# Kernel tuning notes

Measured on AMD Instinct MI355X. Metric: run time of the kernel, lower is better.

Reference implementation:

```python
import jax, jax.numpy as jnp
import numpy as np

N_NODES = 50000
N_EDGES = 800000
H = 128
IN_DIM = 512
N_LAYERS = 3
LN_EPS = 1e-5


def setup_inputs() -> dict:
    key = jax.random.key(0)
    ks = jax.random.split(key, 12)
    s_in = 1.0 / np.sqrt(IN_DIM)
    s_h = 1.0 / np.sqrt(H)
    return {
        "peptide_feature": jax.random.normal(ks[0], (N_NODES, IN_DIM), jnp.float32),
        "proj_W": jax.random.uniform(ks[1], (IN_DIM, H), jnp.float32, -s_in, s_in),
        "proj_b": jax.random.uniform(ks[2], (H,), jnp.float32, -s_in, s_in),
        "edge_emb": jax.random.normal(ks[3], (100, H), jnp.float32),
        "conv_W1": jax.random.uniform(ks[4], (N_LAYERS, H, H), jnp.float32, -s_h, s_h),
        "conv_b1": jax.random.uniform(ks[5], (N_LAYERS, H), jnp.float32, -s_h, s_h),
        "conv_W2": jax.random.uniform(ks[6], (N_LAYERS, H, H), jnp.float32, -s_h, s_h),
        "conv_b2": jax.random.uniform(ks[7], (N_LAYERS, H), jnp.float32, -s_h, s_h),
        "ln_gamma": jnp.ones((H,), jnp.float32),
        "ln_beta": jnp.zeros((H,), jnp.float32),
        "edge_index": jax.random.randint(ks[8], (2, N_EDGES), 0, N_NODES, jnp.int64 if jax.config.jax_enable_x64 else jnp.int32),
        "edge_attr": jax.random.randint(ks[9], (N_EDGES, 1), 0, 100, jnp.int64 if jax.config.jax_enable_x64 else jnp.int32),
    }


def reference(peptide_feature, proj_W, proj_b, edge_emb, conv_W1, conv_b1,
              conv_W2, conv_b2, ln_gamma, ln_beta, edge_index, edge_attr):
    # aanet_proj: Linear(512, H)
    x = peptide_feature @ proj_W + proj_b  # [N, H]
    # edge type embedding lookup
    ea = edge_emb[edge_attr[:, 0]]  # [E, H]
    src, dst = edge_index[0], edge_index[1]
    n = x.shape[0]
    for i in range(N_LAYERS):
        # GINEConv (eps=0): aggr_i = sum_{(j->i)} relu(x_j + e_ji); out = MLP(x + aggr)
        msg = jax.nn.relu(x[src] + ea)  # [E, H] gather + add + relu
        agg = jax.ops.segment_sum(msg, dst, num_segments=n)  # scatter-add [N, H]
        h = x + agg
        h = jax.nn.relu(h @ conv_W1[i] + conv_b1[i]) @ conv_W2[i] + conv_b2[i]
        x = h + x  # residual
    # LayerNorm over last dim
    mu = jnp.mean(x, axis=-1, keepdims=True)
    var = jnp.var(x, axis=-1, keepdims=True)
    return ln_gamma * (x - mu) * jax.lax.rsqrt(var + LN_EPS) + ln_beta
```

## Files before the change

kernel.cpp:

```cpp
#include <hip/hip_runtime.h>
#include <hip/hip_bf16.h>

#define N_NODES 50000
#define N_EDGES 800000
#define H 128
#define IN_DIM 512
#define N_LAYERS 3
#define LN_EPS 1e-5f
#define SCAN_B ((N_NODES + 255) / 256)
#define BIN_CH 8192
#define BIN_BLOCKS ((N_EDGES + BIN_CH - 1) / BIN_CH)

typedef __attribute__((ext_vector_type(4))) float f32x4;
typedef __attribute__((ext_vector_type(8))) short short8;

__device__ inline ushort f2bfu(float f) {
    __hip_bfloat16 h = __float2bfloat16(f);
    return __builtin_bit_cast(ushort, h);
}
__device__ inline float bfu2f(ushort u) {
    uint v = ((uint)u) << 16;
    return __builtin_bit_cast(float, v);
}
__device__ inline float lobf(uint u) { return __builtin_bit_cast(float, u << 16); }
__device__ inline float hibf(uint u) { return __builtin_bit_cast(float, u & 0xffff0000u); }

#define SWZ(row, byte) ((byte) ^ (((row) & 7) << 4))

__device__ inline short8 cvt8(float4 a, float4 b) {
    short8 v;
    v[0] = (short)f2bfu(a.x); v[1] = (short)f2bfu(a.y);
    v[2] = (short)f2bfu(a.z); v[3] = (short)f2bfu(a.w);
    v[4] = (short)f2bfu(b.x); v[5] = (short)f2bfu(b.y);
    v[6] = (short)f2bfu(b.z); v[7] = (short)f2bfu(b.w);
    return v;
}


__global__ void hist_k(const int* __restrict__ dst, int* __restrict__ deg) {
    int e = blockIdx.x * 256 + threadIdx.x;
    if (e < N_EDGES) atomicAdd(&deg[dst[e]], 1);
}

__global__ __launch_bounds__(256) void blocksum_k(const int* __restrict__ deg,
                                                  int* __restrict__ bsum) {
    int i = blockIdx.x * 256 + threadIdx.x;
    int v = (i < N_NODES) ? deg[i] : 0;
    #pragma unroll
    for (int d = 1; d < 64; d <<= 1) v += __shfl_xor(v, d);
    __shared__ int ws[4];
    if ((threadIdx.x & 63) == 0) ws[threadIdx.x >> 6] = v;
    __syncthreads();
    if (threadIdx.x == 0) bsum[blockIdx.x] = ws[0] + ws[1] + ws[2] + ws[3];
}

__global__ __launch_bounds__(256) void scanb_k(const int* __restrict__ bsum,
                                               int* __restrict__ boff) {
    __shared__ int s[256];
    int t = threadIdx.x;
    int v = (t < SCAN_B) ? bsum[t] : 0;
    s[t] = v;
    __syncthreads();
    for (int d = 1; d < 256; d <<= 1) {
        int u = (t >= d) ? s[t - d] : 0;
        __syncthreads();
        s[t] += u;
        __syncthreads();
    }
    boff[t] = s[t] - v;
}

__global__ __launch_bounds__(256) void offs_k(const int* __restrict__ deg,
                                              const int* __restrict__ boff,
                                              int* __restrict__ offs,
                                              int* __restrict__ bbase,
                                              int* __restrict__ bcur) {
    int i = blockIdx.x * 256 + threadIdx.x;
    int lane = threadIdx.x & 63, w = threadIdx.x >> 6;
    int v = (i < N_NODES) ? deg[i] : 0;
    int inc = v;
    #pragma unroll
    for (int d = 1; d < 64; d <<= 1) {
        int u = __shfl_up(inc, d);
        if (lane >= d) inc += u;
    }
    __shared__ int wsum[4];
    if (lane == 63) wsum[w] = inc;
    __syncthreads();
    int wo = 0;
    #pragma unroll
    for (int k = 0; k < 4; k++) if (k < w) wo += wsum[k];
    int exc = boff[blockIdx.x] + wo + inc - v;
    if (i < N_NODES) offs[i] = exc;
    if ((i & 255) == 0 && i < N_NODES) { bbase[i >> 8] = exc; bcur[i >> 8] = exc; }
    if (i == N_NODES - 1) { offs[N_NODES] = exc + v; bbase[SCAN_B] = exc + v; }
}


__global__ __launch_bounds__(256) void binpass_k(const int* __restrict__ src,
                                                 const int* __restrict__ dst,
                                                 const int* __restrict__ attr,
                                                 int* __restrict__ bcur,
                                                 int* __restrict__ tmp_ep,
                                                 ushort* __restrict__ tmp_dst) {
    __shared__ int cnt[SCAN_B];
    __shared__ int lofs[SCAN_B];
    __shared__ int gbase[SCAN_B];
    __shared__ int cnt2[SCAN_B];
    __shared__ int scan_s[256];
    __shared__ int stage_ep[BIN_CH];
    __shared__ ushort stage_dst[BIN_CH];
    int tid = threadIdx.x;
    int e0 = blockIdx.x * BIN_CH;

    if (tid < SCAN_B) { cnt[tid] = 0; cnt2[tid] = 0; }
    __syncthreads();

    #pragma unroll
    for (int k = 0; k < BIN_CH / 256; k++) {
        int e = e0 + k * 256 + tid;
        if (e < N_EDGES) atomicAdd(&cnt[dst[e] >> 8], 1);
    }
    __syncthreads();

    int v = (tid < SCAN_B) ? cnt[tid] : 0;
    scan_s[tid] = v;
    __syncthreads();
    for (int d = 1; d < 256; d <<= 1) {
        int u = (tid >= d) ? scan_s[tid - d] : 0;
        __syncthreads();
        scan_s[tid] += u;
        __syncthreads();
    }
    if (tid < SCAN_B) lofs[tid] = scan_s[tid] - v;
    int total = scan_s[255];

    if (tid < SCAN_B && v > 0) gbase[tid] = atomicAdd(&bcur[tid], v);
    __syncthreads();

    #pragma unroll
    for (int k = 0; k < BIN_CH / 256; k++) {
        int e = e0 + k * 256 + tid;
        if (e < N_EDGES) {
            int d = dst[e];
            int b = d >> 8;
            int loc = lofs[b] + atomicAdd(&cnt2[b], 1);
            stage_ep[loc] = src[e] | (attr[e] << 16);
            stage_dst[loc] = (ushort)d;
        }
    }
    __syncthreads();

    for (int i = tid; i < total; i += 256) {
        ushort d = stage_dst[i];
        int b = d >> 8;
        int gp = gbase[b] + (i - lofs[b]);
        tmp_ep[gp] = stage_ep[i];
        tmp_dst[gp] = d;
    }
}


__global__ __launch_bounds__(256) void finepass_k(const int* __restrict__ tmp_ep,
                                                  const ushort* __restrict__ tmp_dst,
                                                  const int* __restrict__ offs,
                                                  const int* __restrict__ bbase,
                                                  int* __restrict__ epack) {
    __shared__ int cur[256];
    int tid = threadIdx.x;
    int node0 = blockIdx.x << 8;
    int node = node0 + tid;
    cur[tid] = (node < N_NODES) ? offs[node] : 0;
    __syncthreads();
    int lo = bbase[blockIdx.x], hi = bbase[blockIdx.x + 1];
    for (int i = lo + tid; i < hi; i += 256) {
        ushort d = tmp_dst[i];
        int ep = tmp_ep[i];
        int pos = atomicAdd(&cur[d & 255], 1);
        epack[pos] = ep;
    }
}


__global__ __launch_bounds__(256) void prep_w_k(const float* __restrict__ pW,
                                                const float* __restrict__ W1,
                                                const float* __restrict__ W2,
                                                const float* __restrict__ emb,
                                                short* __restrict__ Wt,
                                                short* __restrict__ W1t,
                                                short* __restrict__ W2t,
                                                ushort* __restrict__ embb,
                                                int* __restrict__ deg) {
    int i = blockIdx.x * 256 + threadIdx.x;
    if (i < 128 * 512) {
        int n = i >> 9, k = i & 511;
        Wt[i] = (short)f2bfu(pW[k * 128 + n]);
    }
    if (i < 3 * 128 * 128) {
        int l = i >> 14, rem = i & 16383, n = rem >> 7, k = rem & 127;
        W1t[i] = (short)f2bfu(W1[l * 16384 + k * 128 + n]);
        W2t[i] = (short)f2bfu(W2[l * 16384 + k * 128 + n]);
    }
    if (i < 100 * 128) embb[i] = f2bfu(emb[i]);
    if (i < N_NODES) deg[i] = 0;
}


__global__ __launch_bounds__(512) void proj_k(const float* __restrict__ pep,
                                              const short* __restrict__ Wt,
                                              const float* __restrict__ b,
                                              float* __restrict__ xf,
                                              ushort* __restrict__ xb) {
    __shared__ short SW[128 * 512];
    int tid = threadIdx.x, lane = tid & 63, wid = tid >> 6;

    #pragma unroll
    for (int c = 0; c < 16; c++) {
        int ch = tid + c * 512;
        int row = ch >> 6, kc = (ch & 63) * 16;
        short8 w = *(const short8*)((const char*)Wt + row * 1024 + kc);
        *(short8*)((char*)SW + SWZ(row, row * 1024 + kc)) = w;
    }
    __syncthreads();

    int m0 = blockIdx.x * 256 + wid * 32;

    const float* arow[2];
    #pragma unroll
    for (int mi = 0; mi < 2; mi++) {
        int node = m0 + mi * 16 + (lane & 15);
        if (node > N_NODES - 1) node = N_NODES - 1;
        arow[mi] = pep + (size_t)node * IN_DIM + ((lane >> 4) << 3);
    }

    f32x4 acc[2][8] = {};
    float4 A0[2][2], A1[2][2];
    #pragma unroll
    for (int mi = 0; mi < 2; mi++) {
        A0[mi][0] = *(const float4*)(arow[mi]);
        A0[mi][1] = *(const float4*)(arow[mi] + 4);
        A1[mi][0] = *(const float4*)(arow[mi] + 32);
        A1[mi][1] = *(const float4*)(arow[mi] + 36);
    }

    #pragma unroll
    for (int ks = 0; ks < 16; ks += 2) {
        {
            short8 af0 = cvt8(A0[0][0], A0[0][1]);
            short8 af1 = cvt8(A0[1][0], A0[1][1]);
            if (ks + 2 < 16) {
                #pragma unroll
                for (int mi = 0; mi < 2; mi++) {
                    A0[mi][0] = *(const float4*)(arow[mi] + (ks + 2) * 32);
                    A0[mi][1] = *(const float4*)(arow[mi] + (ks + 2) * 32 + 4);
                }
            }
            int kb2 = (ks * 32 + ((lane >> 4) << 3)) * 2;
            #pragma unroll
            for (int ni = 0; ni < 8; ni++) {
                int n = ni * 16 + (lane & 15);
                short8 bf = *(const short8*)((const char*)SW + SWZ(n, n * 1024 + kb2));
                acc[0][ni] = __builtin_amdgcn_mfma_f32_16x16x32_bf16(af0, bf, acc[0][ni], 0, 0, 0);
                acc[1][ni] = __builtin_amdgcn_mfma_f32_16x16x32_bf16(af1, bf, acc[1][ni], 0, 0, 0);
            }
        }
        {
            short8 af0 = cvt8(A1[0][0], A1[0][1]);
            short8 af1 = cvt8(A1[1][0], A1[1][1]);
            if (ks + 3 < 16) {
                #pragma unroll
                for (int mi = 0; mi < 2; mi++) {
                    A1[mi][0] = *(const float4*)(arow[mi] + (ks + 3) * 32);
                    A1[mi][1] = *(const float4*)(arow[mi] + (ks + 3) * 32 + 4);
                }
            }
            int kb2 = ((ks + 1) * 32 + ((lane >> 4) << 3)) * 2;
            #pragma unroll
            for (int ni = 0; ni < 8; ni++) {
                int n = ni * 16 + (lane & 15);
                short8 bf = *(const short8*)((const char*)SW + SWZ(n, n * 1024 + kb2));
                acc[0][ni] = __builtin_amdgcn_mfma_f32_16x16x32_bf16(af0, bf, acc[0][ni], 0, 0, 0);
                acc[1][ni] = __builtin_amdgcn_mfma_f32_16x16x32_bf16(af1, bf, acc[1][ni], 0, 0, 0);
            }
        }
    }

    #pragma unroll
    for (int ni = 0; ni < 8; ni++) {
        int col = ni * 16 + (lane & 15);
        float bb = b[col];
        #pragma unroll
        for (int mi = 0; mi < 2; mi++) {
            int rowb = m0 + mi * 16 + ((lane >> 4) << 2);
            #pragma unroll
            for (int r = 0; r < 4; r++) {
                int node = rowb + r;
                if (node < N_NODES) {
                    float v = acc[mi][ni][r] + bb;
                    xf[(size_t)node * H + col] = v;
                    xb[(size_t)node * H + col] = f2bfu(v);
                }
            }
        }
    }
}


__global__ __launch_bounds__(256) void gather_k(const ushort* __restrict__ xb,
                                                const int* __restrict__ offs,
                                                const int* __restrict__ epack,
                                                const ushort* __restrict__ embb,
                                                ushort* __restrict__ aggb) {
    int node = (blockIdx.x * 256 + threadIdx.x) >> 6;
    int lane = threadIdx.x & 63;
    if (node >= N_NODES) return;
    int beg = offs[node], end = offs[node + 1];
    float ax = 0.f, ay = 0.f;
    for (int base = beg; base < end; base += 64) {
        int myp = (base + lane < end) ? epack[base + lane] : 0;
        int cnt = min(64, end - base);
        int j = 0;
        for (; j + 4 <= cnt; j += 4) {
            int p0 = __shfl(myp, j), p1 = __shfl(myp, j + 1);
            int p2 = __shfl(myp, j + 2), p3 = __shfl(myp, j + 3);
            uint x0 = *(const uint*)(xb + (size_t)(p0 & 0xffff) * H + lane * 2);
            uint e0 = *(const uint*)(embb + (size_t)(p0 >> 16) * H + lane * 2);
            uint x1 = *(const uint*)(xb + (size_t)(p1 & 0xffff) * H + lane * 2);
            uint e1 = *(const uint*)(embb + (size_t)(p1 >> 16) * H + lane * 2);
            uint x2 = *(const uint*)(xb + (size_t)(p2 & 0xffff) * H + lane * 2);
            uint e2 = *(const uint*)(embb + (size_t)(p2 >> 16) * H + lane * 2);
            uint x3 = *(const uint*)(xb + (size_t)(p3 & 0xffff) * H + lane * 2);
            uint e3 = *(const uint*)(embb + (size_t)(p3 >> 16) * H + lane * 2);
            ax += fmaxf(lobf(x0) + lobf(e0), 0.f);
            ay += fmaxf(hibf(x0) + hibf(e0), 0.f);
            ax += fmaxf(lobf(x1) + lobf(e1), 0.f);
            ay += fmaxf(hibf(x1) + hibf(e1), 0.f);
            ax += fmaxf(lobf(x2) + lobf(e2), 0.f);
            ay += fmaxf(hibf(x2) + hibf(e2), 0.f);
            ax += fmaxf(lobf(x3) + lobf(e3), 0.f);
            ay += fmaxf(hibf(x3) + hibf(e3), 0.f);
        }
        for (; j < cnt; j++) {
            int p = __shfl(myp, j);
            uint xv = *(const uint*)(xb + (size_t)(p & 0xffff) * H + lane * 2);
            uint ev = *(const uint*)(embb + (size_t)(p >> 16) * H + lane * 2);
            ax += fmaxf(lobf(xv) + lobf(ev), 0.f);
            ay += fmaxf(hibf(xv) + hibf(ev), 0.f);
        }
    }
    uint packed = (uint)f2bfu(ax) | ((uint)f2bfu(ay) << 16);
    *(uint*)(aggb + (size_t)node * H + lane * 2) = packed;
}


#define MLP_ROWS 64
__global__ __launch_bounds__(256) void mlp_k(float* __restrict__ xf,
                                             ushort* __restrict__ xb,
                                             const ushort* __restrict__ aggb,
                                             const short* __restrict__ W1t,
                                             const float* __restrict__ b1,
                                             const short* __restrict__ W2t,
                                             const float* __restrict__ b2) {
    __shared__ short S[MLP_ROWS * 128];
    __shared__ short Wb[128 * 128];
    int tid = threadIdx.x, lane = tid & 63, wid = tid >> 6;
    int wr = wid >> 1, wc = wid & 1;
    int m0 = blockIdx.x * MLP_ROWS;

    #pragma unroll
    for (int c = 0; c < 4; c++) {
        int ch = tid + c * 256;
        int row = ch >> 4, k8 = (ch & 15) * 8;
        int node = m0 + row;
        short8 hv;
        if (node < N_NODES) {
            const float* xp = xf + (size_t)node * H + k8;
            float4 x0 = *(const float4*)xp;
            float4 x1 = *(const float4*)(xp + 4);
            short8 ag = *(const short8*)(aggb + (size_t)node * H + k8);
            hv[0] = (short)f2bfu(x0.x + bfu2f((ushort)ag[0]));
            hv[1] = (short)f2bfu(x0.y + bfu2f((ushort)ag[1]));
            hv[2] = (short)f2bfu(x0.z + bfu2f((ushort)ag[2]));
            hv[3] = (short)f2bfu(x0.w + bfu2f((ushort)ag[3]));
            hv[4] = (short)f2bfu(x1.x + bfu2f((ushort)ag[4]));
            hv[5] = (short)f2bfu(x1.y + bfu2f((ushort)ag[5]));
            hv[6] = (short)f2bfu(x1.z + bfu2f((ushort)ag[6]));
            hv[7] = (short)f2bfu(x1.w + bfu2f((ushort)ag[7]));
        } else {
            hv = (short8)0;
        }
        *(short8*)((char*)S + SWZ(row, row * 256 + k8 * 2)) = hv;
    }
    #pragma unroll
    for (int c = 0; c < 8; c++) {
        int ch = tid + c * 256;
        int row = ch >> 4, k8 = (ch & 15) * 8;
        short8 w = *(const short8*)(W1t + row * H + k8);
        *(short8*)((char*)Wb + SWZ(row, row * 256 + k8 * 2)) = w;
    }
    short8 wreg2[8];
    #pragma unroll
    for (int c = 0; c < 8; c++) {
        int ch = tid + c * 256;
        int row = ch >> 4, k8 = (ch & 15) * 8;
        wreg2[c] = *(const short8*)(W2t + row * H + k8);
    }
    __syncthreads();

    f32x4 a1[2][4] = {};
    #pragma unroll
    for (int ks = 0; ks < 4; ks++) {
        int kb = ks * 32 + (lane >> 4) * 8;
        short8 af[2], bfr[4];
        #pragma unroll
        for (int mi = 0; mi < 2; mi++) {
            int r = wr * 32 + mi * 16 + (lane & 15);
            af[mi] = *(const short8*)((const char*)S + SWZ(r, r * 256 + kb * 2));
        }
        #pragma unroll
        for (int ni = 0; ni < 4; ni++) {
            int n = wc * 64 + ni * 16 + (lane & 15);
            bfr[ni] = *(const short8*)((const char*)Wb + SWZ(n, n * 256 + kb * 2));
        }
        #pragma unroll
        for (int mi = 0; mi < 2; mi++)
            #pragma unroll
            for (int ni = 0; ni < 4; ni++)
                a1[mi][ni] = __builtin_amdgcn_mfma_f32_16x16x32_bf16(
                    af[mi], bfr[ni], a1[mi][ni], 0, 0, 0);
    }
    __syncthreads();

    #pragma unroll
    for (int ni = 0; ni < 4; ni++) {
        int n = wc * 64 + ni * 16 + (lane & 15);
        float bb = b1[n];
        #pragma unroll
        for (int mi = 0; mi < 2; mi++) {
            int mrow = wr * 32 + mi * 16 + ((lane >> 4) << 2);
            #pragma unroll
            for (int r = 0; r < 4; r++) {
                int m = mrow + r;
                float tv = fmaxf(a1[mi][ni][r] + bb, 0.f);
                *(ushort*)((char*)S + SWZ(m, m * 256 + n * 2)) = f2bfu(tv);
            }
        }
    }
    #pragma unroll
    for (int c = 0; c < 8; c++) {
        int ch = tid + c * 256;
        int row = ch >> 4, k8 = (ch & 15) * 8;
        *(short8*)((char*)Wb + SWZ(row, row * 256 + k8 * 2)) = wreg2[c];
    }
    __syncthreads();

    f32x4 a2[4][2] = {};
    #pragma unroll
    for (int ks = 0; ks < 4; ks++) {
        int kb = ks * 32 + (lane >> 4) * 8;
        short8 af[4], bfr[2];
        #pragma unroll
        for (int mi = 0; mi < 4; mi++) {
            int n2 = wr * 64 + mi * 16 + (lane & 15);
            af[mi] = *(const short8*)((const char*)Wb + SWZ(n2, n2 * 256 + kb * 2));
        }
        #pragma unroll
        for (int ni = 0; ni < 2; ni++) {
            int m = wc * 32 + ni * 16 + (lane & 15);
            bfr[ni] = *(const short8*)((const char*)S + SWZ(m, m * 256 + kb * 2));
        }
        #pragma unroll
        for (int mi = 0; mi < 4; mi++)
            #pragma unroll
            for (int ni = 0; ni < 2; ni++)
                a2[mi][ni] = __builtin_amdgcn_mfma_f32_16x16x32_bf16(
                    af[mi], bfr[ni], a2[mi][ni], 0, 0, 0);
    }

    #pragma unroll
    for (int ni = 0; ni < 2; ni++) {
        int node = m0 + wc * 32 + ni * 16 + (lane & 15);
        if (node >= N_NODES) continue;
        #pragma unroll
        for (int mi = 0; mi < 4; mi++) {
            int n2b = wr * 64 + mi * 16 + ((lane >> 4) << 2);
            float4 xo = *(float4*)(xf + (size_t)node * H + n2b);
            float4 bb = *(const float4*)(b2 + n2b);
            float4 o;
            o.x = a2[mi][ni][0] + bb.x + xo.x;
            o.y = a2[mi][ni][1] + bb.y + xo.y;
            o.z = a2[mi][ni][2] + bb.z + xo.z;
            o.w = a2[mi][ni][3] + bb.w + xo.w;
            *(float4*)(xf + (size_t)node * H + n2b) = o;
            ushort us[4] = {f2bfu(o.x), f2bfu(o.y), f2bfu(o.z), f2bfu(o.w)};
            *(ulong*)(xb + (size_t)node * H + n2b) = *(ulong*)us;
        }
    }
}


__global__ __launch_bounds__(256) void ln_k(const float* __restrict__ x,
                                            const float* __restrict__ gamma,
                                            const float* __restrict__ beta,
                                            float* __restrict__ out) {
    int node = (blockIdx.x * 256 + threadIdx.x) >> 6;
    int lane = threadIdx.x & 63;
    if (node >= N_NODES) return;
    float2 v = ((const float2*)(x + (size_t)node * H))[lane];
    float s = v.x + v.y;
    #pragma unroll
    for (int d = 1; d < 64; d <<= 1) s += __shfl_xor(s, d);
    float mu = s * (1.f / 128.f);
    float dx = v.x - mu, dy = v.y - mu;
    float q = dx * dx + dy * dy;
    #pragma unroll
    for (int d = 1; d < 64; d <<= 1) q += __shfl_xor(q, d);
    float inv = rsqrtf(q * (1.f / 128.f) + LN_EPS);
    float2 gm = ((const float2*)gamma)[lane];
    float2 bt = ((const float2*)beta)[lane];
    float2 o;
    o.x = gm.x * dx * inv + bt.x;
    o.y = gm.y * dy * inv + bt.y;
    ((float2*)(out + (size_t)node * H))[lane] = o;
}


extern "C" void kernel_launch(void* const* d_in, const int* in_sizes, int n_in,
                              void* d_out, int out_size, void* d_ws, size_t ws_size,
                              hipStream_t stream) {
    const float* pep    = (const float*)d_in[0];
    const float* proj_W = (const float*)d_in[1];
    const float* proj_b = (const float*)d_in[2];
    const float* emb    = (const float*)d_in[3];
    const float* cW1    = (const float*)d_in[4];
    const float* cb1    = (const float*)d_in[5];
    const float* cW2    = (const float*)d_in[6];
    const float* cb2    = (const float*)d_in[7];
    const float* gamma  = (const float*)d_in[8];
    const float* beta   = (const float*)d_in[9];
    const int*   eidx   = (const int*)d_in[10];
    const int*   attr   = (const int*)d_in[11];
    const int* src = eidx;
    const int* dst = eidx + N_EDGES;

    char* w = (char*)d_ws;
    float*  xf    = (float*)w;              w += (size_t)N_NODES * H * 4;
    ushort* xb    = (ushort*)w;             w += (size_t)N_NODES * H * 2;
    ushort* aggb  = (ushort*)w;             w += (size_t)N_NODES * H * 2;
    short*  Wt    = (short*)w;              w += 128 * 512 * 2;
    short*  W1t   = (short*)w;              w += 3 * 128 * 128 * 2;
    short*  W2t   = (short*)w;              w += 3 * 128 * 128 * 2;
    ushort* embb  = (ushort*)w;             w += 100 * 128 * 2;
    int*    offs  = (int*)w;                w += (N_NODES + 16) * 4;
    int*    deg   = (int*)w;                w += (N_NODES + 16) * 4;
    int*    bsum  = (int*)w;                w += 256 * 4;
    int*    boff  = (int*)w;                w += 256 * 4;
    int*    bbase = (int*)w;                w += 256 * 4;
    int*    bcur  = (int*)w;                w += 256 * 4;
    int*    epack = (int*)w;                w += (size_t)N_EDGES * 4;
    int*    tmp_ep = (int*)w;               w += (size_t)N_EDGES * 4;
    ushort* tmp_dst = (ushort*)w;           w += (size_t)N_EDGES * 2;

    float* out = (float*)d_out;

    prep_w_k<<<256, 256, 0, stream>>>(proj_W, cW1, cW2, emb, Wt, W1t, W2t, embb, deg);
    hist_k<<<(N_EDGES + 255) / 256, 256, 0, stream>>>(dst, deg);
    blocksum_k<<<SCAN_B, 256, 0, stream>>>(deg, bsum);
    scanb_k<<<1, 256, 0, stream>>>(bsum, boff);
    offs_k<<<SCAN_B, 256, 0, stream>>>(deg, boff, offs, bbase, bcur);
    binpass_k<<<BIN_BLOCKS, 256, 0, stream>>>(src, dst, attr, bcur, tmp_ep, tmp_dst);
    finepass_k<<<SCAN_B, 256, 0, stream>>>(tmp_ep, tmp_dst, offs, bbase, epack);

    proj_k<<<(N_NODES + 255) / 256, 512, 0, stream>>>(pep, Wt, proj_b, xf, xb);

    for (int l = 0; l < N_LAYERS; l++) {
        gather_k<<<(N_NODES * 64 + 255) / 256, 256, 0, stream>>>(
            xb, offs, epack, embb, aggb);
        mlp_k<<<(N_NODES + MLP_ROWS - 1) / MLP_ROWS, 256, 0, stream>>>(
            xf, xb, aggb,
            W1t + (size_t)l * H * H, cb1 + (size_t)l * H,
            W2t + (size_t)l * H * H, cb2 + (size_t)l * H);
    }

    ln_k<<<(N_NODES * 64 + 255) / 256, 256, 0, stream>>>(xf, gamma, beta, out);
}
```

Measured before the change: 305.5 us.

## Fuse neighbor gather-aggregation into MLP kernel with ping-pong bf16 buffers

Removes the separate gather kernel. Each MLP block now gathers and aggregates its own 64 nodes' neighbor messages and writes x+agg straight into shared memory, which avoids the round trip of the aggregate buffer through global memory and one launch per layer. Because other blocks still read the bf16 features of the current layer, the bf16 copy is double-buffered, and the final layer skips writing it. The cost is less parallelism for the irregular gather: one wave handles 16 nodes serially inside an MLP block with large shared memory, so occupancy and latency hiding for the gather may drop.

Measured after the change: 477.4 us. 56.3% more time.

```diff
diff --git a/kernel.cpp b/kernel.cpp
--- a/kernel.cpp
+++ b/kernel.cpp
@@ -306,61 +306,18 @@
 }
 
 
-__global__ __launch_bounds__(256) void gather_k(const ushort* __restrict__ xb,
-                                                const int* __restrict__ offs,
-                                                const int* __restrict__ epack,
-                                                const ushort* __restrict__ embb,
-                                                ushort* __restrict__ aggb) {
-    int node = (blockIdx.x * 256 + threadIdx.x) >> 6;
-    int lane = threadIdx.x & 63;
-    if (node >= N_NODES) return;
-    int beg = offs[node], end = offs[node + 1];
-    float ax = 0.f, ay = 0.f;
-    for (int base = beg; base < end; base += 64) {
-        int myp = (base + lane < end) ? epack[base + lane] : 0;
-        int cnt = min(64, end - base);
-        int j = 0;
-        for (; j + 4 <= cnt; j += 4) {
-            int p0 = __shfl(myp, j), p1 = __shfl(myp, j + 1);
-            int p2 = __shfl(myp, j + 2), p3 = __shfl(myp, j + 3);
-            uint x0 = *(const uint*)(xb + (size_t)(p0 & 0xffff) * H + lane * 2);
-            uint e0 = *(const uint*)(embb + (size_t)(p0 >> 16) * H + lane * 2);
-            uint x1 = *(const uint*)(xb + (size_t)(p1 & 0xffff) * H + lane * 2);
-            uint e1 = *(const uint*)(embb + (size_t)(p1 >> 16) * H + lane * 2);
-            uint x2 = *(const uint*)(xb + (size_t)(p2 & 0xffff) * H + lane * 2);
-            uint e2 = *(const uint*)(embb + (size_t)(p2 >> 16) * H + lane * 2);
-            uint x3 = *(const uint*)(xb + (size_t)(p3 & 0xffff) * H + lane * 2);
-            uint e3 = *(const uint*)(embb + (size_t)(p3 >> 16) * H + lane * 2);
-            ax += fmaxf(lobf(x0) + lobf(e0), 0.f);
-            ay += fmaxf(hibf(x0) + hibf(e0), 0.f);
-            ax += fmaxf(lobf(x1) + lobf(e1), 0.f);
-            ay += fmaxf(hibf(x1) + hibf(e1), 0.f);
-            ax += fmaxf(lobf(x2) + lobf(e2), 0.f);
-            ay += fmaxf(hibf(x2) + hibf(e2), 0.f);
-            ax += fmaxf(lobf(x3) + lobf(e3), 0.f);
-            ay += fmaxf(hibf(x3) + hibf(e3), 0.f);
-        }
-        for (; j < cnt; j++) {
-            int p = __shfl(myp, j);
-            uint xv = *(const uint*)(xb + (size_t)(p & 0xffff) * H + lane * 2);
-            uint ev = *(const uint*)(embb + (size_t)(p >> 16) * H + lane * 2);
-            ax += fmaxf(lobf(xv) + lobf(ev), 0.f);
-            ay += fmaxf(hibf(xv) + hibf(ev), 0.f);
-        }
-    }
-    uint packed = (uint)f2bfu(ax) | ((uint)f2bfu(ay) << 16);
-    *(uint*)(aggb + (size_t)node * H + lane * 2) = packed;
-}
-
-
 #define MLP_ROWS 64
 __global__ __launch_bounds__(256) void mlp_k(float* __restrict__ xf,
-                                             ushort* __restrict__ xb,
-                                             const ushort* __restrict__ aggb,
+                                             const ushort* __restrict__ xb_in,
+                                             ushort* __restrict__ xb_out,
+                                             const int* __restrict__ offs,
+                                             const int* __restrict__ epack,
+                                             const ushort* __restrict__ embb,
                                              const short* __restrict__ W1t,
                                              const float* __restrict__ b1,
                                              const short* __restrict__ W2t,
-                                             const float* __restrict__ b2) {
+                                             const float* __restrict__ b2,
+                                             int write_xb) {
     __shared__ short S[MLP_ROWS * 128];
     __shared__ short Wb[128 * 128];
     int tid = threadIdx.x, lane = tid & 63, wid = tid >> 6;
@@ -368,30 +325,6 @@
     int m0 = blockIdx.x * MLP_ROWS;
 
     #pragma unroll
-    for (int c = 0; c < 4; c++) {
-        int ch = tid + c * 256;
-        int row = ch >> 4, k8 = (ch & 15) * 8;
-        int node = m0 + row;
-        short8 hv;
-        if (node < N_NODES) {
-            const float* xp = xf + (size_t)node * H + k8;
-            float4 x0 = *(const float4*)xp;
-            float4 x1 = *(const float4*)(xp + 4);
-            short8 ag = *(const short8*)(aggb + (size_t)node * H + k8);
-            hv[0] = (short)f2bfu(x0.x + bfu2f((ushort)ag[0]));
-            hv[1] = (short)f2bfu(x0.y + bfu2f((ushort)ag[1]));
-            hv[2] = (short)f2bfu(x0.z + bfu2f((ushort)ag[2]));
-            hv[3] = (short)f2bfu(x0.w + bfu2f((ushort)ag[3]));
-            hv[4] = (short)f2bfu(x1.x + bfu2f((ushort)ag[4]));
-            hv[5] = (short)f2bfu(x1.y + bfu2f((ushort)ag[5]));
-            hv[6] = (short)f2bfu(x1.z + bfu2f((ushort)ag[6]));
-            hv[7] = (short)f2bfu(x1.w + bfu2f((ushort)ag[7]));
-        } else {
-            hv = (short8)0;
-        }
-        *(short8*)((char*)S + SWZ(row, row * 256 + k8 * 2)) = hv;
-    }
-    #pragma unroll
     for (int c = 0; c < 8; c++) {
         int ch = tid + c * 256;
         int row = ch >> 4, k8 = (ch & 15) * 8;
@@ -404,6 +337,51 @@
         int ch = tid + c * 256;
         int row = ch >> 4, k8 = (ch & 15) * 8;
         wreg2[c] = *(const short8*)(W2t + row * H + k8);
+    }
+
+    for (int i = 0; i < 16; i++) {
+        int row = wid * 16 + i;
+        int node = m0 + row;
+        uint hp = 0;
+        if (node < N_NODES) {
+            int beg = offs[node], end = offs[node + 1];
+            float ax = 0.f, ay = 0.f;
+            for (int base = beg; base < end; base += 64) {
+                int myp = (base + lane < end) ? epack[base + lane] : 0;
+                int cnt = min(64, end - base);
+                int j = 0;
+                for (; j + 4 <= cnt; j += 4) {
+                    int p0 = __shfl(myp, j), p1 = __shfl(myp, j + 1);
+                    int p2 = __shfl(myp, j + 2), p3 = __shfl(myp, j + 3);
+                    uint x0 = *(const uint*)(xb_in + (size_t)(p0 & 0xffff) * H + lane * 2);
+                    uint e0 = *(const uint*)(embb + (size_t)(p0 >> 16) * H + lane * 2);
+                    uint x1 = *(const uint*)(xb_in + (size_t)(p1 & 0xffff) * H + lane * 2);
+                    uint e1 = *(const uint*)(embb + (size_t)(p1 >> 16) * H + lane * 2);
+                    uint x2 = *(const uint*)(xb_in + (size_t)(p2 & 0xffff) * H + lane * 2);
+                    uint e2 = *(const uint*)(embb + (size_t)(p2 >> 16) * H + lane * 2);
+                    uint x3 = *(const uint*)(xb_in + (size_t)(p3 & 0xffff) * H + lane * 2);
+                    uint e3 = *(const uint*)(embb + (size_t)(p3 >> 16) * H + lane * 2);
+                    ax += fmaxf(lobf(x0) + lobf(e0), 0.f);
+                    ay += fmaxf(hibf(x0) + hibf(e0), 0.f);
+                    ax += fmaxf(lobf(x1) + lobf(e1), 0.f);
+                    ay += fmaxf(hibf(x1) + hibf(e1), 0.f);
+                    ax += fmaxf(lobf(x2) + lobf(e2), 0.f);
+                    ay += fmaxf(hibf(x2) + hibf(e2), 0.f);
+                    ax += fmaxf(lobf(x3) + lobf(e3), 0.f);
+                    ay += fmaxf(hibf(x3) + hibf(e3), 0.f);
+                }
+                for (; j < cnt; j++) {
+                    int p = __shfl(myp, j);
+                    uint xv = *(const uint*)(xb_in + (size_t)(p & 0xffff) * H + lane * 2);
+                    uint ev = *(const uint*)(embb + (size_t)(p >> 16) * H + lane * 2);
+                    ax += fmaxf(lobf(xv) + lobf(ev), 0.f);
+                    ay += fmaxf(hibf(xv) + hibf(ev), 0.f);
+                }
+            }
+            float2 vx = ((const float2*)(xf + (size_t)node * H))[lane];
+            hp = (uint)f2bfu(vx.x + ax) | ((uint)f2bfu(vx.y + ay) << 16);
+        }
+        *(uint*)((char*)S + SWZ(row, row * 256 + lane * 4)) = hp;
     }
     __syncthreads();
 
@@ -492,8 +470,10 @@
             o.z = a2[mi][ni][2] + bb.z + xo.z;
             o.w = a2[mi][ni][3] + bb.w + xo.w;
             *(float4*)(xf + (size_t)node * H + n2b) = o;
-            ushort us[4] = {f2bfu(o.x), f2bfu(o.y), f2bfu(o.z), f2bfu(o.w)};
-            *(ulong*)(xb + (size_t)node * H + n2b) = *(ulong*)us;
+            if (write_xb) {
+                ushort us[4] = {f2bfu(o.x), f2bfu(o.y), f2bfu(o.z), f2bfu(o.w)};
+                *(ulong*)(xb_out + (size_t)node * H + n2b) = *(ulong*)us;
+            }
         }
     }
 }
@@ -545,8 +525,8 @@
 
     char* w = (char*)d_ws;
     float*  xf    = (float*)w;              w += (size_t)N_NODES * H * 4;
-    ushort* xb    = (ushort*)w;             w += (size_t)N_NODES * H * 2;
-    ushort* aggb  = (ushort*)w;             w += (size_t)N_NODES * H * 2;
+    ushort* xb0   = (ushort*)w;             w += (size_t)N_NODES * H * 2;
+    ushort* xb1   = (ushort*)w;             w += (size_t)N_NODES * H * 2;
     short*  Wt    = (short*)w;              w += 128 * 512 * 2;
     short*  W1t   = (short*)w;              w += 3 * 128 * 128 * 2;
     short*  W2t   = (short*)w;              w += 3 * 128 * 128 * 2;
@@ -571,15 +551,15 @@
     binpass_k<<<BIN_BLOCKS, 256, 0, stream>>>(src, dst, attr, bcur, tmp_ep, tmp_dst);
     finepass_k<<<SCAN_B, 256, 0, stream>>>(tmp_ep, tmp_dst, offs, bbase, epack);
 
-    proj_k<<<(N_NODES + 255) / 256, 512, 0, stream>>>(pep, Wt, proj_b, xf, xb);
-
+    proj_k<<<(N_NODES + 255) / 256, 512, 0, stream>>>(pep, Wt, proj_b, xf, xb0);
+
+    ushort* xbuf[2] = {xb0, xb1};
     for (int l = 0; l < N_LAYERS; l++) {
-        gather_k<<<(N_NODES * 64 + 255) / 256, 256, 0, stream>>>(
-            xb, offs, epack, embb, aggb);
         mlp_k<<<(N_NODES + MLP_ROWS - 1) / MLP_ROWS, 256, 0, stream>>>(
-            xf, xb, aggb,
+            xf, xbuf[l & 1], xbuf[(l + 1) & 1], offs, epack, embb,
             W1t + (size_t)l * H * H, cb1 + (size_t)l * H,
-            W2t + (size_t)l * H * H, cb2 + (size_t)l * H);
+            W2t + (size_t)l * H * H, cb2 + (size_t)l * H,
+            (l < N_LAYERS - 1) ? 1 : 0);
     }
 
     ln_k<<<(N_NODES * 64 + 255) / 256, 256, 0, stream>>>(xf, gamma, beta, out);
```
